# Kernel tuning notes

Hardware: AMD Instinct MI355X
Metric: run time of the kernel (lower is better)

Reference implementation:

```python
import jax, jax.numpy as jnp
import numpy as np
from jax.ops import segment_sum

N = 100000   # nodes
E = 1600000  # edges
D = 128      # node_feature_dim == hidden_dim
DE = 16      # edge_feature_dim
G = 512      # num_graphs
EPS = 1e-5   # BatchNorm eps


def setup_inputs() -> dict:
    key = jax.random.key(0)
    ks = jax.random.split(key, 24)
    inp = {
        "x": jax.random.normal(ks[0], (N, D), jnp.float32),
        "edge_index": jax.random.randint(ks[1], (2, E), 0, N, jnp.int64),
        "batch_idx": jnp.sort(jax.random.randint(ks[2], (N,), 0, G, jnp.int64)),
        "edge_attr": jax.random.normal(ks[3], (E, DE), jnp.float32),
        "num_graphs": G,
    }
    s = 1.0 / np.sqrt(D)
    # GCN layer 1 (D -> D) + BatchNorm1d (eval-mode running stats)
    inp["W1"] = jax.random.normal(ks[4], (D, D), jnp.float32) * s
    inp["b1"] = jnp.zeros((D,), jnp.float32)
    inp["g1"] = jax.random.uniform(ks[5], (D,), jnp.float32, 0.5, 1.5)
    inp["bt1"] = jax.random.normal(ks[6], (D,), jnp.float32) * 0.1
    inp["m1"] = jax.random.normal(ks[7], (D,), jnp.float32) * 0.1
    inp["v1"] = jax.random.uniform(ks[8], (D,), jnp.float32, 0.5, 1.5)
    # GCN layer 2
    inp["W2"] = jax.random.normal(ks[9], (D, D), jnp.float32) * s
    inp["b2"] = jnp.zeros((D,), jnp.float32)
    inp["g2"] = jax.random.uniform(ks[10], (D,), jnp.float32, 0.5, 1.5)
    inp["bt2"] = jax.random.normal(ks[11], (D,), jnp.float32) * 0.1
    inp["m2"] = jax.random.normal(ks[12], (D,), jnp.float32) * 0.1
    inp["v2"] = jax.random.uniform(ks[13], (D,), jnp.float32, 0.5, 1.5)
    # edge encoder: Linear(DE,D) -> ReLU -> Linear(D,D)
    inp["We1"] = jax.random.normal(ks[14], (DE, D), jnp.float32) / np.sqrt(DE)
    inp["be1"] = jnp.zeros((D,), jnp.float32)
    inp["We2"] = jax.random.normal(ks[15], (D, D), jnp.float32) * s
    inp["be2"] = jnp.zeros((D,), jnp.float32)
    return inp


def _gcn_conv(x, W, b, src, dst, n):
    # PyG GCNConv: add self-loops, sym norm D^-1/2 (A+I) D^-1/2, then X W + b
    xw = x @ W  # [n, out]
    loops = jnp.arange(n, dtype=src.dtype)
    s = jnp.concatenate([src, loops])
    d = jnp.concatenate([dst, loops])
    deg = segment_sum(jnp.ones_like(d, dtype=xw.dtype), d, num_segments=n)
    dinv = jnp.where(deg > 0, jax.lax.rsqrt(jnp.maximum(deg, 1.0)), 0.0)
    norm = dinv[s] * dinv[d]  # [e+n]
    msg = xw[s] * norm[:, None]
    return segment_sum(msg, d, num_segments=n) + b


def _bn_relu(x, g, bt, m, v):
    return jax.nn.relu((x - m) * jax.lax.rsqrt(v + EPS) * g + bt)


def reference(x, edge_index, batch_idx, edge_attr, num_graphs,
              W1, b1, g1, bt1, m1, v1,
              W2, b2, g2, bt2, m2, v2,
              We1, be1, We2, be2):
    n = x.shape[0]
    src, dst = edge_index[0], edge_index[1]
    # two GraphConvLayer: GCNConv -> BN(eval) -> ReLU -> Dropout(eval=id)
    h = _bn_relu(_gcn_conv(x, W1, b1, src, dst, n), g1, bt1, m1, v1)
    h = _bn_relu(_gcn_conv(h, W2, b2, src, dst, n), g2, bt2, m2, v2)
    # global mean pool over nodes per graph
    nsum = segment_sum(h, batch_idx, num_segments=num_graphs)
    ncnt = segment_sum(jnp.ones((n,), h.dtype), batch_idx, num_segments=num_graphs)
    graph_repr = nsum / jnp.maximum(ncnt, 1.0)[:, None]
    # edge encoder + per-graph edge mean (fused segment-mean)
    e = jax.nn.relu(edge_attr @ We1 + be1) @ We2 + be2  # [E, D]
    edge_batch = batch_idx[src]
    esum = segment_sum(e, edge_batch, num_segments=num_graphs)
    ecnt = segment_sum(jnp.ones((e.shape[0],), e.dtype), edge_batch, num_segments=num_graphs)
    edge_repr = jnp.where(ecnt[:, None] > 0, esum / jnp.maximum(ecnt, 1.0)[:, None], 0.0)
    return graph_repr + edge_repr
```

## Files before the change

kernel.cpp:

```cpp
#include <hip/hip_runtime.h>

#define N_NODES 100000
#define N_EDGES 1600000
#define D 128
#define DE 16
#define G 512
#define EPSBN 1e-5f
#define ESLICE 4
#define EPB 1024
#define EPT (EPB / 256)
#define SCHUNK 1024
#define NSB ((N_NODES + SCHUNK - 1) / SCHUNK)
#define AGG_CH 16
#define DSHIFT 9
#define DBSZ 512
#define NBKT ((N_NODES + DBSZ - 1) / DBSZ)

typedef __bf16 bf16x8 __attribute__((ext_vector_type(8)));
typedef __bf16 bf16x4 __attribute__((ext_vector_type(4)));
typedef float f32x4 __attribute__((ext_vector_type(4)));

__device__ __forceinline__ float bf_lo(unsigned v) { return __uint_as_float(v << 16); }
__device__ __forceinline__ float bf_hi(unsigned v) { return __uint_as_float(v & 0xffff0000u); }

__global__ void k_init(int* __restrict__ deg, int* __restrict__ ecnt, int* __restrict__ dcnt,
                       float* __restrict__ gcnt, float* __restrict__ gsum,
                       float* __restrict__ esum) {
  int i = blockIdx.x * 256 + threadIdx.x;
  if (i < N_NODES) deg[i] = 1;
  if (i < G) { ecnt[i] = 0; gcnt[i] = 0.f; }
  if (i < NBKT) dcnt[i] = 0;
  if (i < G * D) { gsum[i] = 0.f; esum[i] = 0.f; }
}

__global__ void k_count(const int* __restrict__ ei, const int* __restrict__ batch,
                        int* __restrict__ deg, int* __restrict__ ecnt, int* __restrict__ dcnt) {
  __shared__ int bins[G];
  __shared__ int dbins[NBKT];
  int tid = threadIdx.x;
  for (int i = tid; i < G; i += 256) bins[i] = 0;
  for (int i = tid; i < NBKT; i += 256) dbins[i] = 0;
  __syncthreads();
  int base = blockIdx.x * 4096;
  for (int t = tid; t < 4096; t += 256) {
    int e = base + t;
    if (e < N_EDGES) {
      int s = ei[e];
      int d = ei[N_EDGES + e];
      atomicAdd(&deg[d], 1);
      atomicAdd(&bins[batch[s]], 1);
      atomicAdd(&dbins[d >> DSHIFT], 1);
    }
  }
  __syncthreads();
  for (int i = tid; i < G; i += 256) if (bins[i]) atomicAdd(&ecnt[i], bins[i]);
  for (int i = tid; i < NBKT; i += 256) if (dbins[i]) atomicAdd(&dcnt[i], dbins[i]);
}

__global__ __launch_bounds__(256) void k_scan_part(const int* __restrict__ deg,
                                                   int* __restrict__ part) {
  __shared__ int red[4];
  int tid = threadIdx.x;
  int base = blockIdx.x * SCHUNK + tid * 4;
  int s = 0;
  #pragma unroll
  for (int k = 0; k < 4; ++k) {
    int i = base + k;
    if (i < N_NODES) s += deg[i];
  }
  #pragma unroll
  for (int off = 32; off > 0; off >>= 1) s += __shfl_down(s, off);
  if ((tid & 63) == 0) red[tid >> 6] = s;
  __syncthreads();
  if (tid == 0) part[blockIdx.x] = red[0] + red[1] + red[2] + red[3];
}

__global__ void k_scan_mid(int* __restrict__ part, const int* __restrict__ ecnt,
                           int* __restrict__ ebs, int* __restrict__ ecur_pad,
                           const int* __restrict__ dcnt, int* __restrict__ dbs,
                           int* __restrict__ dcur_pad) {
  __shared__ int sb[512];
  int tid = threadIdx.x;
  int v = (tid < NSB) ? part[tid] : 0;
  sb[tid] = v;
  __syncthreads();
  for (int off = 1; off < 512; off <<= 1) {
    int t = (tid >= off) ? sb[tid - off] : 0;
    __syncthreads();
    sb[tid] += t;
    __syncthreads();
  }
  if (tid < NSB) part[tid] = sb[tid] - v;
  __syncthreads();
  int v2 = ecnt[tid];
  sb[tid] = v2;
  __syncthreads();
  for (int off = 1; off < 512; off <<= 1) {
    int t = (tid >= off) ? sb[tid - off] : 0;
    __syncthreads();
    sb[tid] += t;
    __syncthreads();
  }
  ebs[tid] = sb[tid] - v2;
  ecur_pad[tid * 16] = sb[tid] - v2;
  __syncthreads();
  int v3 = (tid < NBKT) ? dcnt[tid] : 0;
  sb[tid] = v3;
  __syncthreads();
  for (int off = 1; off < 512; off <<= 1) {
    int t = (tid >= off) ? sb[tid - off] : 0;
    __syncthreads();
    sb[tid] += t;
    __syncthreads();
  }
  if (tid < NBKT) { dbs[tid] = sb[tid] - v3; dcur_pad[tid * 16] = sb[tid] - v3; }
}

__global__ __launch_bounds__(256) void k_scan_write(const int* __restrict__ deg,
                                                    const int* __restrict__ part,
                                                    int* __restrict__ rs,
                                                    float* __restrict__ dinv) {
  __shared__ int sb[256];
  int tid = threadIdx.x;
  int base = blockIdx.x * SCHUNK + tid * 4;
  int d[4];
  int s = 0;
  #pragma unroll
  for (int k = 0; k < 4; ++k) {
    int i = base + k;
    d[k] = (i < N_NODES) ? deg[i] : 0;
    s += d[k];
  }
  sb[tid] = s;
  __syncthreads();
  for (int off = 1; off < 256; off <<= 1) {
    int t = (tid >= off) ? sb[tid - off] : 0;
    __syncthreads();
    sb[tid] += t;
    __syncthreads();
  }
  int ex = sb[tid] - s + part[blockIdx.x];
  #pragma unroll
  for (int k = 0; k < 4; ++k) {
    int i = base + k;
    if (i < N_NODES) {
      rs[i] = ex;
      dinv[i] = rsqrtf((float)d[k]);
      ex += d[k];
    }
  }
}

__global__ __launch_bounds__(256) void k_scatter(const int* __restrict__ ei,
                                                 const int* __restrict__ batch,
                                                 int* __restrict__ ecur_pad,
                                                 int* __restrict__ dcur_pad,
                                                 int2* __restrict__ pairs,
                                                 int* __restrict__ idlist) {
  __shared__ int gbins[G];
  __shared__ int gbase[G];
  __shared__ int dbins[NBKT];
  __shared__ int dbase[NBKT];
  __shared__ int gsrc[EPB];
  __shared__ int gdst[EPB];
  __shared__ int dsrc[EPB];
  __shared__ int ddst[EPB];
  int tid = threadIdx.x;
  for (int i = tid; i < G; i += 256) gbins[i] = 0;
  for (int i = tid; i < NBKT; i += 256) dbins[i] = 0;
  __syncthreads();
  int e0 = blockIdx.x * EPB;
  int nvalid = N_EDGES - e0;
  if (nvalid > EPB) nvalid = EPB;
  int ge[EPT], gr[EPT], db[EPT], dr[EPT];
  #pragma unroll
  for (int k = 0; k < EPT; ++k) {
    int e = e0 + k * 256 + tid;
    ge[k] = -1;
    if (e < N_EDGES) {
      int s = ei[e], d = ei[N_EDGES + e];
      int g = batch[s];
      ge[k] = g;
      gr[k] = atomicAdd(&gbins[g], 1);
      db[k] = d >> DSHIFT;
      dr[k] = atomicAdd(&dbins[db[k]], 1);
    }
  }
  __syncthreads();
  for (int i = tid; i < G; i += 256) {
    int cnt = gbins[i];
    gbase[i] = cnt ? atomicAdd(&ecur_pad[i * 16], cnt) : 0;
  }
  for (int i = tid; i < NBKT; i += 256) {
    int cnt = dbins[i];
    dbase[i] = cnt ? atomicAdd(&dcur_pad[i * 16], cnt) : 0;
  }
  int v0 = gbins[tid], v1 = gbins[tid + 256];
  int vd = (tid < NBKT) ? dbins[tid] : 0;
  gsrc[tid] = vd;
  __syncthreads();
  for (int off = 1; off < 512; off <<= 1) {
    int a = (tid >= off) ? gbins[tid - off] : 0;
    int b = gbins[tid + 256 - off];
    int c = (off < 256 && tid >= off) ? gsrc[tid - off] : 0;
    __syncthreads();
    gbins[tid] += a;
    gbins[tid + 256] += b;
    if (off < 256) gsrc[tid] += c;
    __syncthreads();
  }
  gbins[tid] -= v0;
  gbins[tid + 256] -= v1;
  if (tid < NBKT) dbins[tid] = gsrc[tid] - vd;
  __syncthreads();
  #pragma unroll
  for (int k = 0; k < EPT; ++k) {
    if (ge[k] >= 0) {
      int el = k * 256 + tid;
      int g = ge[k];
      int sG = gbins[g] + gr[k];
      gsrc[sG] = el;
      gdst[sG] = gbase[g] + gr[k];
      int bkt = db[k];
      int sD = dbins[bkt] + dr[k];
      dsrc[sD] = el;
      ddst[sD] = dbase[bkt] + dr[k];
    }
  }
  __syncthreads();
  for (int p = tid; p < nvalid; p += 256) {
    idlist[gdst[p]] = e0 + gsrc[p];
  }
  for (int p = tid; p < nvalid; p += 256) {
    int e = e0 + dsrc[p];
    pairs[ddst[p]] = make_int2(ei[e], ei[N_EDGES + e]);
  }
}

__global__ __launch_bounds__(256) void k_scatter_nbr(const int2* __restrict__ pairs,
                                                     const int* __restrict__ dbs,
                                                     const int* __restrict__ dcnt,
                                                     const int* __restrict__ rs,
                                                     int* __restrict__ nbr) {
  __shared__ int cur[DBSZ];
  int tid = threadIdx.x;
  int bkt = blockIdx.x;
  int nodeBase = bkt << DSHIFT;
  for (int l = tid; l < DBSZ; l += 256) {
    int node = nodeBase + l;
    cur[l] = (node < N_NODES) ? rs[node] : 0;
  }
  __syncthreads();
  int start = dbs[bkt], n = dcnt[bkt];
  for (int i = tid; i < n; i += 256) {
    int2 p = pairs[start + i];
    int pos = atomicAdd(&cur[p.y - nodeBase], 1);
    nbr[pos] = p.x;
  }
}

__global__ void k_prep_w(const float* __restrict__ W, __bf16* __restrict__ Wf) {
  int tid = threadIdx.x;
  for (int idx = blockIdx.x * 256 + tid; idx < 16384; idx += 8 * 256) {
    int j = idx & 7;
    int lane = (idx >> 3) & 63;
    int cb = (idx >> 9) & 7;
    int kc = idx >> 12;
    int k = kc * 32 + (lane >> 4) * 8 + j;
    int n = cb * 16 + (lane & 15);
    Wf[idx] = (__bf16)W[k * 128 + n];
  }
}

__global__ __launch_bounds__(256) void k_gemm_mfma(const float* __restrict__ X,
                                                   const __bf16* __restrict__ Wf,
                                                   const float* __restrict__ dinv,
                                                   __bf16* __restrict__ out) {
  __shared__ __bf16 sXb[64][136];
  int tid = threadIdx.x;
  int wave = tid >> 6, lane = tid & 63;
  int m = lane & 15, kg = lane >> 4;
  int base = blockIdx.x * 64;
  #pragma unroll
  for (int i = 0; i < 8; ++i) {
    int idx = tid + i * 256;
    int r = idx >> 5, cq = idx & 31;
    int row = base + r;
    float4 v = make_float4(0.f, 0.f, 0.f, 0.f);
    if (row < N_NODES) v = *(const float4*)(X + (size_t)row * 128 + cq * 4);
    bf16x4 h;
    h[0] = (__bf16)v.x; h[1] = (__bf16)v.y; h[2] = (__bf16)v.z; h[3] = (__bf16)v.w;
    *(bf16x4*)(&sXb[r][cq * 4]) = h;
  }
  __syncthreads();
  int r0 = wave * 16;
  f32x4 acc[8];
  #pragma unroll
  for (int cb = 0; cb < 8; ++cb) acc[cb] = (f32x4){0.f, 0.f, 0.f, 0.f};
  #pragma unroll
  for (int kc = 0; kc < 4; ++kc) {
    bf16x8 afrag = *(const bf16x8*)(&sXb[r0 + m][kc * 32 + kg * 8]);
    #pragma unroll
    for (int cb = 0; cb < 8; ++cb) {
      bf16x8 bfrag = *(const bf16x8*)(Wf + (((size_t)(kc * 8 + cb) * 64 + lane) << 3));
      acc[cb] = __builtin_amdgcn_mfma_f32_16x16x32_bf16(afrag, bfrag, acc[cb], 0, 0, 0);
    }
  }
  #pragma unroll
  for (int r = 0; r < 4; ++r) {
    int grow = base + r0 + kg * 4 + r;
    if (grow < N_NODES) {
      float dv = dinv[grow];
      #pragma unroll
      for (int cb = 0; cb < 8; ++cb)
        out[(size_t)grow * 128 + cb * 16 + m] = (__bf16)(acc[cb][r] * dv);
    }
  }
}

__global__ __launch_bounds__(256) void k_agg_bn(const unsigned* __restrict__ Au,
                                                const int* __restrict__ nbr,
                                                const int* __restrict__ rs,
                                                const int* __restrict__ deg,
                                                const float* __restrict__ dinv,
                                                const float* __restrict__ b,
                                                const float* __restrict__ gm,
                                                const float* __restrict__ bt,
                                                const float* __restrict__ m,
                                                const float* __restrict__ v,
                                                float* __restrict__ outB) {
  int tid = threadIdx.x;
  int wave = tid >> 6, lane = tid & 63;
  int c0 = lane * 2, c1 = c0 + 1;
  float sc0 = gm[c0] * rsqrtf(v[c0] + EPSBN), sc1 = gm[c1] * rsqrtf(v[c1] + EPSBN);
  float sh0 = bt[c0] - m[c0] * sc0, sh1 = bt[c1] - m[c1] * sc1;
  float bb0 = b[c0], bb1 = b[c1];
  int base = (blockIdx.x * 4 + wave) * AGG_CH;
  for (int nn = 0; nn < AGG_CH; ++nn) {
    int i = base + nn;
    if (i >= N_NODES) return;
    unsigned sv = Au[(size_t)i * 64 + lane];
    float s0 = bf_lo(sv), s1 = bf_hi(sv);
    int j = rs[i];
    int end = j + deg[i] - 1;
    for (; j + 3 < end; j += 4) {
      int n0 = nbr[j], n1 = nbr[j + 1], n2 = nbr[j + 2], n3 = nbr[j + 3];
      unsigned a0 = Au[(size_t)n0 * 64 + lane];
      unsigned a1 = Au[(size_t)n1 * 64 + lane];
      unsigned a2 = Au[(size_t)n2 * 64 + lane];
      unsigned a3 = Au[(size_t)n3 * 64 + lane];
      s0 += bf_lo(a0) + bf_lo(a1) + bf_lo(a2) + bf_lo(a3);
      s1 += bf_hi(a0) + bf_hi(a1) + bf_hi(a2) + bf_hi(a3);
    }
    for (; j < end; ++j) {
      unsigned a = Au[(size_t)nbr[j] * 64 + lane];
      s0 += bf_lo(a); s1 += bf_hi(a);
    }
    float dv = dinv[i];
    float y0 = fmaxf((dv * s0 + bb0) * sc0 + sh0, 0.f);
    float y1 = fmaxf((dv * s1 + bb1) * sc1 + sh1, 0.f);
    *(float2*)(outB + (size_t)i * 128 + c0) = make_float2(y0, y1);
  }
}

__global__ __launch_bounds__(256) void k_agg_bn_pool(const unsigned* __restrict__ Au,
                                                     const int* __restrict__ nbr,
                                                     const int* __restrict__ rs,
                                                     const int* __restrict__ deg,
                                                     const float* __restrict__ dinv,
                                                     const int* __restrict__ batch,
                                                     const float* __restrict__ b,
                                                     const float* __restrict__ gm,
                                                     const float* __restrict__ bt,
                                                     const float* __restrict__ m,
                                                     const float* __restrict__ v,
                                                     float* __restrict__ gsum,
                                                     float* __restrict__ gcnt) {
  int tid = threadIdx.x;
  int wave = tid >> 6, lane = tid & 63;
  int c0 = lane * 2, c1 = c0 + 1;
  float sc0 = gm[c0] * rsqrtf(v[c0] + EPSBN), sc1 = gm[c1] * rsqrtf(v[c1] + EPSBN);
  float sh0 = bt[c0] - m[c0] * sc0, sh1 = bt[c1] - m[c1] * sc1;
  float bb0 = b[c0], bb1 = b[c1];
  int base = (blockIdx.x * 4 + wave) * AGG_CH;
  if (base >= N_NODES) return;
  float acc0 = 0.f, acc1 = 0.f, cnt = 0.f;
  int curg = -1;
  for (int nn = 0; nn < AGG_CH; ++nn) {
    int i = base + nn;
    if (i >= N_NODES) break;
    int bg = batch[i];
    if (bg != curg) {
      if (curg >= 0) {
        atomicAdd(&gsum[(size_t)curg * 128 + c0], acc0);
        atomicAdd(&gsum[(size_t)curg * 128 + c1], acc1);
        if (lane == 0) atomicAdd(&gcnt[curg], cnt);
      }
      acc0 = 0.f; acc1 = 0.f; cnt = 0.f; curg = bg;
    }
    unsigned sv = Au[(size_t)i * 64 + lane];
    float s0 = bf_lo(sv), s1 = bf_hi(sv);
    int j = rs[i];
    int end = j + deg[i] - 1;
    for (; j + 3 < end; j += 4) {
      int n0 = nbr[j], n1 = nbr[j + 1], n2 = nbr[j + 2], n3 = nbr[j + 3];
      unsigned a0 = Au[(size_t)n0 * 64 + lane];
      unsigned a1 = Au[(size_t)n1 * 64 + lane];
      unsigned a2 = Au[(size_t)n2 * 64 + lane];
      unsigned a3 = Au[(size_t)n3 * 64 + lane];
      s0 += bf_lo(a0) + bf_lo(a1) + bf_lo(a2) + bf_lo(a3);
      s1 += bf_hi(a0) + bf_hi(a1) + bf_hi(a2) + bf_hi(a3);
    }
    for (; j < end; ++j) {
      unsigned a = Au[(size_t)nbr[j] * 64 + lane];
      s0 += bf_lo(a); s1 += bf_hi(a);
    }
    float dv = dinv[i];
    acc0 += fmaxf((dv * s0 + bb0) * sc0 + sh0, 0.f);
    acc1 += fmaxf((dv * s1 + bb1) * sc1 + sh1, 0.f);
    cnt += 1.f;
  }
  if (curg >= 0) {
    atomicAdd(&gsum[(size_t)curg * 128 + c0], acc0);
    atomicAdd(&gsum[(size_t)curg * 128 + c1], acc1);
    if (lane == 0) atomicAdd(&gcnt[curg], cnt);
  }
}

__global__ __launch_bounds__(256) void k_edge_hidden(
    const float* __restrict__ edge_attr,
    const int* __restrict__ idlist,
    const int* __restrict__ ebs, const int* __restrict__ ecnt,
    const float* __restrict__ We1, const float* __restrict__ be1,
    float* __restrict__ esum) {
  int tid = threadIdx.x;
  int wave = tid >> 6;
  int lane = tid & 63;
  int n = lane & 15;
  int kg = lane >> 4;
  int toff = kg >> 1;
  int cp = kg & 1;
  int g = blockIdx.x / ESLICE;
  int slice = blockIdx.x % ESLICE;

  bf16x8 bfrag[8];
  float biasv[8];
  #pragma unroll
  for (int blk = 0; blk < 8; ++blk) {
    #pragma unroll
    for (int j = 0; j < 8; ++j) {
      int k = kg * 8 + j;
      float w = (k < DE) ? We1[k * 128 + blk * 16 + n] : 0.f;
      bfrag[blk][j] = (__bf16)w;
    }
    biasv[blk] = be1[blk * 16 + n];
  }

  int start = ebs[g], cnt = ecnt[g];
  int lim = start + cnt;
  int ntiles = (cnt + 15) >> 4;
  const int nstream = ESLICE * 4;
  int sid = slice * 4 + wave;
  int tpc = (ntiles + nstream - 1) / nstream;
  int t0 = sid * tpc;
  int t1 = t0 + tpc; if (t1 > ntiles) t1 = ntiles;

  float racc[8] = {0.f, 0.f, 0.f, 0.f, 0.f, 0.f, 0.f, 0.f};

  auto compute_tile = [&](int t, bf16x8 afrag) {
    int jb = start + (t << 4);
    if (jb + 16 <= lim) {
      #pragma unroll
      for (int blk = 0; blk < 8; ++blk) {
        f32x4 acc = {0.f, 0.f, 0.f, 0.f};
        acc = __builtin_amdgcn_mfma_f32_16x16x32_bf16(afrag, bfrag[blk], acc, 0, 0, 0);
        #pragma unroll
        for (int r = 0; r < 4; ++r)
          racc[blk] += fmaxf(acc[r] + biasv[blk], 0.f);
      }
    } else {
      #pragma unroll
      for (int blk = 0; blk < 8; ++blk) {
        f32x4 acc = {0.f, 0.f, 0.f, 0.f};
        acc = __builtin_amdgcn_mfma_f32_16x16x32_bf16(afrag, bfrag[blk], acc, 0, 0, 0);
        #pragma unroll
        for (int r = 0; r < 4; ++r) {
          int rr = kg * 4 + r;
          if (jb + rr < lim) racc[blk] += fmaxf(acc[r] + biasv[blk], 0.f);
        }
      }
    }
  };

  for (int t = t0; t < t1; t += 2) {
    int tt = t + toff;
    int ttc = tt < ntiles ? tt : ntiles - 1;
    int slot = start + (ttc << 4) + n;
    int sc = slot < lim - 1 ? slot : lim - 1;
    int e = idlist[sc];
    const float4* q = (const float4*)(edge_attr + (size_t)e * DE + cp * 8);
    float4 f0 = q[0], f1 = q[1];
    union { bf16x8 v; int i[4]; } mine, swp;
    mine.v[0] = (__bf16)f0.x; mine.v[1] = (__bf16)f0.y;
    mine.v[2] = (__bf16)f0.z; mine.v[3] = (__bf16)f0.w;
    mine.v[4] = (__bf16)f1.x; mine.v[5] = (__bf16)f1.y;
    mine.v[6] = (__bf16)f1.z; mine.v[7] = (__bf16)f1.w;
    #pragma unroll
    for (int w2 = 0; w2 < 4; ++w2) swp.i[w2] = __shfl_xor(mine.i[w2], 32);
    bf16x8 a0 = {}, a1 = {};
    if (kg < 2) { a0 = mine.v; a1 = swp.v; }
    compute_tile(t, a0);
    if (t + 1 < t1) compute_tile(t + 1, a1);
  }

  #pragma unroll
  for (int blk = 0; blk < 8; ++blk) {
    float vsum = racc[blk];
    vsum += __shfl_xor(vsum, 16);
    vsum += __shfl_xor(vsum, 32);
    if (lane < 16) atomicAdd(&esum[(size_t)g * 128 + blk * 16 + n], vsum);
  }
}

__global__ void k_final(const float* __restrict__ esum, const int* __restrict__ ecnt,
                        const float* __restrict__ gsum, const float* __restrict__ gcnt,
                        const float* __restrict__ We2, const float* __restrict__ be2,
                        float* __restrict__ out) {
  __shared__ float mh[128];
  int g = blockIdx.x, c = threadIdx.x;
  int ec = ecnt[g];
  mh[c] = (ec > 0) ? esum[(size_t)g * 128 + c] / (float)ec : 0.f;
  __syncthreads();
  float acc = 0.f;
  #pragma unroll 8
  for (int k = 0; k < 128; ++k) acc += mh[k] * We2[k * 128 + c];
  float er = (ec > 0) ? (acc + be2[c]) : 0.f;
  float gr = gsum[(size_t)g * 128 + c] / fmaxf(gcnt[g], 1.f);
  out[(size_t)g * 128 + c] = gr + er;
}

extern "C" void kernel_launch(void* const* d_in, const int* in_sizes, int n_in,
                              void* d_out, int out_size, void* d_ws, size_t ws_size,
                              hipStream_t stream) {
  const float* x        = (const float*)d_in[0];
  const int*   ei       = (const int*)d_in[1];
  const int*   batch    = (const int*)d_in[2];
  const float* edge_attr= (const float*)d_in[3];
  const float* W1 = (const float*)d_in[5];
  const float* b1 = (const float*)d_in[6];
  const float* g1 = (const float*)d_in[7];
  const float* bt1= (const float*)d_in[8];
  const float* m1 = (const float*)d_in[9];
  const float* v1 = (const float*)d_in[10];
  const float* W2 = (const float*)d_in[11];
  const float* b2 = (const float*)d_in[12];
  const float* g2 = (const float*)d_in[13];
  const float* bt2= (const float*)d_in[14];
  const float* m2 = (const float*)d_in[15];
  const float* v2 = (const float*)d_in[16];
  const float* We1= (const float*)d_in[17];
  const float* be1= (const float*)d_in[18];
  const float* We2= (const float*)d_in[19];
  const float* be2= (const float*)d_in[20];
  float* out = (float*)d_out;

  char* ws = (char*)d_ws;
  size_t off = 0;
  auto take = [&](size_t bytes) -> char* {
    char* p = ws + off;
    off += (bytes + 255) & ~(size_t)255;
    return p;
  };
  __bf16* A       = (__bf16*)take((size_t)N_NODES * 128 * 2);
  float*  B       = (float*) take((size_t)N_NODES * 128 * 4);
  float*  dinv    = (float*) take((size_t)N_NODES * 4);
  int*    deg     = (int*)   take((size_t)N_NODES * 4);
  int*    rs      = (int*)   take((size_t)N_NODES * 4);
  int*    nbr     = (int*)   take((size_t)(N_EDGES + N_NODES) * 4);
  int2*   pairs   = (int2*)  take((size_t)N_EDGES * 8);
  int*    idlist  = (int*)   take((size_t)N_EDGES * 4);
  __bf16* Wf1     = (__bf16*)take((size_t)16384 * 2);
  __bf16* Wf2     = (__bf16*)take((size_t)16384 * 2);
  int*    ecnt    = (int*)   take((size_t)G * 4);
  int*    ebs     = (int*)   take((size_t)G * 4);
  int*    ecur_pad= (int*)   take((size_t)G * 16 * 4);
  int*    dcnt    = (int*)   take((size_t)NBKT * 4);
  int*    dbs     = (int*)   take((size_t)NBKT * 4);
  int*    dcur_pad= (int*)   take((size_t)NBKT * 16 * 4);
  float*  gcnt    = (float*) take((size_t)G * 4);
  float*  esum    = (float*) take((size_t)G * 128 * 4);
  float*  gsum    = (float*) take((size_t)G * 128 * 4);
  int*    part    = (int*)   take((size_t)NSB * 4);

  k_init<<<(N_NODES + 255) / 256, 256, 0, stream>>>(deg, ecnt, dcnt, gcnt, gsum, esum);
  k_prep_w<<<8, 256, 0, stream>>>(W1, Wf1);
  k_prep_w<<<8, 256, 0, stream>>>(W2, Wf2);
  k_count<<<(N_EDGES + 4095) / 4096, 256, 0, stream>>>(ei, batch, deg, ecnt, dcnt);
  k_scan_part<<<NSB, 256, 0, stream>>>(deg, part);
  k_scan_mid<<<1, 512, 0, stream>>>(part, ecnt, ebs, ecur_pad, dcnt, dbs, dcur_pad);
  k_scan_write<<<NSB, 256, 0, stream>>>(deg, part, rs, dinv);
  k_scatter<<<(N_EDGES + EPB - 1) / EPB, 256, 0, stream>>>(ei, batch, ecur_pad, dcur_pad, pairs, idlist);
  k_scatter_nbr<<<NBKT, 256, 0, stream>>>(pairs, dbs, dcnt, rs, nbr);
  const int aggBlocks = (N_NODES + 4 * AGG_CH - 1) / (4 * AGG_CH);
  k_gemm_mfma<<<(N_NODES + 63) / 64, 256, 0, stream>>>(x, Wf1, dinv, A);
  k_agg_bn<<<aggBlocks, 256, 0, stream>>>((const unsigned*)A, nbr, rs, deg, dinv, b1, g1, bt1, m1, v1, B);
  k_gemm_mfma<<<(N_NODES + 63) / 64, 256, 0, stream>>>(B, Wf2, dinv, A);
  k_agg_bn_pool<<<aggBlocks, 256, 0, stream>>>((const unsigned*)A, nbr, rs, deg, dinv, batch, b2, g2, bt2, m2, v2, gsum, gcnt);
  k_edge_hidden<<<G * ESLICE, 256, 0, stream>>>(edge_attr, idlist, ebs, ecnt, We1, be1, esum);
  k_final<<<G, 128, 0, stream>>>(esum, ecnt, gsum, gcnt, We2, be2, out);
}
```

Measured before the change: 693.6 us.

## Co-schedule edge encoder blocks with the two aggregation kernels

The standalone edge-hidden kernel is split into two halves, and each half is appended as extra blocks to the layer-1 and layer-2 aggregation launches, dispatched by block index. This lets the compute-bound MFMA edge encoding overlap with the memory-bound neighbor gathers and removes one kernel launch. The combined kernels may use more registers, since the launch bound is shared by both bodies, which could lower occupancy for the gather blocks.

```diff
diff --git a/kernel.cpp b/kernel.cpp
--- a/kernel.cpp
+++ b/kernel.cpp
@@ -12,6 +12,7 @@
 #define SCHUNK 1024
 #define NSB ((N_NODES + SCHUNK - 1) / SCHUNK)
 #define AGG_CH 16
+#define AGGB ((N_NODES + 4 * AGG_CH - 1) / (4 * AGG_CH))
 #define DSHIFT 9
 #define DBSZ 512
 #define NBKT ((N_NODES + DBSZ - 1) / DBSZ)
@@ -318,24 +319,21 @@
   }
 }
 
-__global__ __launch_bounds__(256) void k_agg_bn(const unsigned* __restrict__ Au,
-                                                const int* __restrict__ nbr,
-                                                const int* __restrict__ rs,
-                                                const int* __restrict__ deg,
-                                                const float* __restrict__ dinv,
-                                                const float* __restrict__ b,
-                                                const float* __restrict__ gm,
-                                                const float* __restrict__ bt,
-                                                const float* __restrict__ m,
-                                                const float* __restrict__ v,
-                                                float* __restrict__ outB) {
+
+__device__ __forceinline__ void agg_bn_body(
+    int blk, const unsigned* __restrict__ Au, const int* __restrict__ nbr,
+    const int* __restrict__ rs, const int* __restrict__ deg,
+    const float* __restrict__ dinv, const float* __restrict__ b,
+    const float* __restrict__ gm, const float* __restrict__ bt,
+    const float* __restrict__ m, const float* __restrict__ v,
+    float* __restrict__ outB) {
   int tid = threadIdx.x;
   int wave = tid >> 6, lane = tid & 63;
   int c0 = lane * 2, c1 = c0 + 1;
   float sc0 = gm[c0] * rsqrtf(v[c0] + EPSBN), sc1 = gm[c1] * rsqrtf(v[c1] + EPSBN);
   float sh0 = bt[c0] - m[c0] * sc0, sh1 = bt[c1] - m[c1] * sc1;
   float bb0 = b[c0], bb1 = b[c1];
-  int base = (blockIdx.x * 4 + wave) * AGG_CH;
+  int base = (blk * 4 + wave) * AGG_CH;
   for (int nn = 0; nn < AGG_CH; ++nn) {
     int i = base + nn;
     if (i >= N_NODES) return;
@@ -363,26 +361,21 @@
   }
 }
 
-__global__ __launch_bounds__(256) void k_agg_bn_pool(const unsigned* __restrict__ Au,
-                                                     const int* __restrict__ nbr,
-                                                     const int* __restrict__ rs,
-                                                     const int* __restrict__ deg,
-                                                     const float* __restrict__ dinv,
-                                                     const int* __restrict__ batch,
-                                                     const float* __restrict__ b,
-                                                     const float* __restrict__ gm,
-                                                     const float* __restrict__ bt,
-                                                     const float* __restrict__ m,
-                                                     const float* __restrict__ v,
-                                                     float* __restrict__ gsum,
-                                                     float* __restrict__ gcnt) {
+__device__ __forceinline__ void agg_bn_pool_body(
+    int blk, const unsigned* __restrict__ Au, const int* __restrict__ nbr,
+    const int* __restrict__ rs, const int* __restrict__ deg,
+    const float* __restrict__ dinv, const int* __restrict__ batch,
+    const float* __restrict__ b, const float* __restrict__ gm,
+    const float* __restrict__ bt, const float* __restrict__ m,
+    const float* __restrict__ v, float* __restrict__ gsum,
+    float* __restrict__ gcnt) {
   int tid = threadIdx.x;
   int wave = tid >> 6, lane = tid & 63;
   int c0 = lane * 2, c1 = c0 + 1;
   float sc0 = gm[c0] * rsqrtf(v[c0] + EPSBN), sc1 = gm[c1] * rsqrtf(v[c1] + EPSBN);
   float sh0 = bt[c0] - m[c0] * sc0, sh1 = bt[c1] - m[c1] * sc1;
   float bb0 = b[c0], bb1 = b[c1];
-  int base = (blockIdx.x * 4 + wave) * AGG_CH;
+  int base = (blk * 4 + wave) * AGG_CH;
   if (base >= N_NODES) return;
   float acc0 = 0.f, acc1 = 0.f, cnt = 0.f;
   int curg = -1;
@@ -427,12 +420,11 @@
   }
 }
 
-__global__ __launch_bounds__(256) void k_edge_hidden(
-    const float* __restrict__ edge_attr,
-    const int* __restrict__ idlist,
-    const int* __restrict__ ebs, const int* __restrict__ ecnt,
-    const float* __restrict__ We1, const float* __restrict__ be1,
-    float* __restrict__ esum) {
+__device__ __forceinline__ void edge_hidden_body(
+    int g, int slice, const float* __restrict__ edge_attr,
+    const int* __restrict__ idlist, const int* __restrict__ ebs,
+    const int* __restrict__ ecnt, const float* __restrict__ We1,
+    const float* __restrict__ be1, float* __restrict__ esum) {
   int tid = threadIdx.x;
   int wave = tid >> 6;
   int lane = tid & 63;
@@ -440,8 +432,6 @@
   int kg = lane >> 4;
   int toff = kg >> 1;
   int cp = kg & 1;
-  int g = blockIdx.x / ESLICE;
-  int slice = blockIdx.x % ESLICE;
 
   bf16x8 bfrag[8];
   float biasv[8];
@@ -519,6 +509,47 @@
     vsum += __shfl_xor(vsum, 16);
     vsum += __shfl_xor(vsum, 32);
     if (lane < 16) atomicAdd(&esum[(size_t)g * 128 + blk * 16 + n], vsum);
+  }
+}
+
+__global__ __launch_bounds__(256) void k_fused_l1(
+    const unsigned* __restrict__ Au, const int* __restrict__ nbr,
+    const int* __restrict__ rs, const int* __restrict__ deg,
+    const float* __restrict__ dinv, const float* __restrict__ b,
+    const float* __restrict__ gm, const float* __restrict__ bt,
+    const float* __restrict__ m, const float* __restrict__ v,
+    float* __restrict__ outB,
+    const float* __restrict__ edge_attr, const int* __restrict__ idlist,
+    const int* __restrict__ ebs, const int* __restrict__ ecnt,
+    const float* __restrict__ We1, const float* __restrict__ be1,
+    float* __restrict__ esum) {
+  int bid = blockIdx.x;
+  if (bid < AGGB) {
+    agg_bn_body(bid, Au, nbr, rs, deg, dinv, b, gm, bt, m, v, outB);
+  } else {
+    int eb = bid - AGGB;
+    edge_hidden_body(eb >> 1, eb & 1, edge_attr, idlist, ebs, ecnt, We1, be1, esum);
+  }
+}
+
+__global__ __launch_bounds__(256) void k_fused_l2(
+    const unsigned* __restrict__ Au, const int* __restrict__ nbr,
+    const int* __restrict__ rs, const int* __restrict__ deg,
+    const float* __restrict__ dinv, const int* __restrict__ batch,
+    const float* __restrict__ b, const float* __restrict__ gm,
+    const float* __restrict__ bt, const float* __restrict__ m,
+    const float* __restrict__ v, float* __restrict__ gsum,
+    float* __restrict__ gcnt,
+    const float* __restrict__ edge_attr, const int* __restrict__ idlist,
+    const int* __restrict__ ebs, const int* __restrict__ ecnt,
+    const float* __restrict__ We1, const float* __restrict__ be1,
+    float* __restrict__ esum) {
+  int bid = blockIdx.x;
+  if (bid < AGGB) {
+    agg_bn_pool_body(bid, Au, nbr, rs, deg, dinv, batch, b, gm, bt, m, v, gsum, gcnt);
+  } else {
+    int eb = bid - AGGB;
+    edge_hidden_body(eb >> 1, 2 + (eb & 1), edge_attr, idlist, ebs, ecnt, We1, be1, esum);
   }
 }
 
@@ -601,11 +632,13 @@
   k_scan_write<<<NSB, 256, 0, stream>>>(deg, part, rs, dinv);
   k_scatter<<<(N_EDGES + EPB - 1) / EPB, 256, 0, stream>>>(ei, batch, ecur_pad, dcur_pad, pairs, idlist);
   k_scatter_nbr<<<NBKT, 256, 0, stream>>>(pairs, dbs, dcnt, rs, nbr);
-  const int aggBlocks = (N_NODES + 4 * AGG_CH - 1) / (4 * AGG_CH);
   k_gemm_mfma<<<(N_NODES + 63) / 64, 256, 0, stream>>>(x, Wf1, dinv, A);
-  k_agg_bn<<<aggBlocks, 256, 0, stream>>>((const unsigned*)A, nbr, rs, deg, dinv, b1, g1, bt1, m1, v1, B);
+  k_fused_l1<<<AGGB + 2 * G, 256, 0, stream>>>((const unsigned*)A, nbr, rs, deg, dinv,
+                                               b1, g1, bt1, m1, v1, B,
+                                               edge_attr, idlist, ebs, ecnt, We1, be1, esum);
   k_gemm_mfma<<<(N_NODES + 63) / 64, 256, 0, stream>>>(B, Wf2, dinv, A);
-  k_agg_bn_pool<<<aggBlocks, 256, 0, stream>>>((const unsigned*)A, nbr, rs, deg, dinv, batch, b2, g2, bt2, m2, v2, gsum, gcnt);
-  k_edge_hidden<<<G * ESLICE, 256, 0, stream>>>(edge_attr, idlist, ebs, ecnt, We1, be1, esum);
+  k_fused_l2<<<AGGB + 2 * G, 256, 0, stream>>>((const unsigned*)A, nbr, rs, deg, dinv, batch,
+                                               b2, g2, bt2, m2, v2, gsum, gcnt,
+                                               edge_attr, idlist, ebs, ecnt, We1, be1, esum);
   k_final<<<G, 128, 0, stream>>>(esum, ecnt, gsum, gcnt, We2, be2, out);
 }
```

Measured after the change: 835.0 us. 1.2x slower.

## Pre-convert edge features to bf16 in count pass and merge setup kernels

Applied to the files above, without the earlier changes.

Edge attributes are now converted to bf16 once, in the streaming count kernel, and stored in a new workspace buffer. The edge-hidden kernel then gathers 16-byte bf16 rows instead of 32-byte fp32 rows for its random idlist accesses, and the lane-to-row mapping is rearranged so each lane loads one half row. The init and the two weight-prep launches are merged into a single setup kernel to cut launch count. The cost is an extra 51 MB write plus a full read of edge_attr in the count kernel.

```diff
diff --git a/kernel.cpp b/kernel.cpp
--- a/kernel.cpp
+++ b/kernel.cpp
@@ -15,6 +15,7 @@
 #define DSHIFT 9
 #define DBSZ 512
 #define NBKT ((N_NODES + DBSZ - 1) / DBSZ)
+#define INITB ((N_NODES + 255) / 256)
 
 typedef __bf16 bf16x8 __attribute__((ext_vector_type(8)));
 typedef __bf16 bf16x4 __attribute__((ext_vector_type(4)));
@@ -23,17 +24,41 @@
 __device__ __forceinline__ float bf_lo(unsigned v) { return __uint_as_float(v << 16); }
 __device__ __forceinline__ float bf_hi(unsigned v) { return __uint_as_float(v & 0xffff0000u); }
 
-__global__ void k_init(int* __restrict__ deg, int* __restrict__ ecnt, int* __restrict__ dcnt,
-                       float* __restrict__ gcnt, float* __restrict__ gsum,
-                       float* __restrict__ esum) {
-  int i = blockIdx.x * 256 + threadIdx.x;
-  if (i < N_NODES) deg[i] = 1;
-  if (i < G) { ecnt[i] = 0; gcnt[i] = 0.f; }
-  if (i < NBKT) dcnt[i] = 0;
-  if (i < G * D) { gsum[i] = 0.f; esum[i] = 0.f; }
+__device__ __forceinline__ void prep_w_body(int pb, const float* __restrict__ W,
+                                            __bf16* __restrict__ Wf) {
+  int tid = threadIdx.x;
+  for (int idx = pb * 256 + tid; idx < 16384; idx += 8 * 256) {
+    int j = idx & 7;
+    int lane = (idx >> 3) & 63;
+    int cb = (idx >> 9) & 7;
+    int kc = idx >> 12;
+    int k = kc * 32 + (lane >> 4) * 8 + j;
+    int n = cb * 16 + (lane & 15);
+    Wf[idx] = (__bf16)W[k * 128 + n];
+  }
+}
+
+__global__ void k_setup(int* __restrict__ deg, int* __restrict__ ecnt, int* __restrict__ dcnt,
+                        float* __restrict__ gcnt, float* __restrict__ gsum,
+                        float* __restrict__ esum,
+                        const float* __restrict__ W1, __bf16* __restrict__ Wf1,
+                        const float* __restrict__ W2, __bf16* __restrict__ Wf2) {
+  int b = blockIdx.x;
+  if (b < INITB) {
+    int i = b * 256 + threadIdx.x;
+    if (i < N_NODES) deg[i] = 1;
+    if (i < G) { ecnt[i] = 0; gcnt[i] = 0.f; }
+    if (i < NBKT) dcnt[i] = 0;
+    if (i < G * D) { gsum[i] = 0.f; esum[i] = 0.f; }
+  } else if (b < INITB + 8) {
+    prep_w_body(b - INITB, W1, Wf1);
+  } else {
+    prep_w_body(b - INITB - 8, W2, Wf2);
+  }
 }
 
 __global__ void k_count(const int* __restrict__ ei, const int* __restrict__ batch,
+                        const float* __restrict__ edge_attr, __bf16* __restrict__ eaB,
                         int* __restrict__ deg, int* __restrict__ ecnt, int* __restrict__ dcnt) {
   __shared__ int bins[G];
   __shared__ int dbins[NBKT];
@@ -50,6 +75,15 @@
       atomicAdd(&deg[d], 1);
       atomicAdd(&bins[batch[s]], 1);
       atomicAdd(&dbins[d >> DSHIFT], 1);
+      const float4* p = (const float4*)(edge_attr + (size_t)e * DE);
+      float4 f0 = p[0], f1 = p[1], f2 = p[2], f3 = p[3];
+      bf16x8 h0, h1;
+      h0[0] = (__bf16)f0.x; h0[1] = (__bf16)f0.y; h0[2] = (__bf16)f0.z; h0[3] = (__bf16)f0.w;
+      h0[4] = (__bf16)f1.x; h0[5] = (__bf16)f1.y; h0[6] = (__bf16)f1.z; h0[7] = (__bf16)f1.w;
+      h1[0] = (__bf16)f2.x; h1[1] = (__bf16)f2.y; h1[2] = (__bf16)f2.z; h1[3] = (__bf16)f2.w;
+      h1[4] = (__bf16)f3.x; h1[5] = (__bf16)f3.y; h1[6] = (__bf16)f3.z; h1[7] = (__bf16)f3.w;
+      bf16x8* q = (bf16x8*)(eaB + (size_t)e * DE);
+      q[0] = h0; q[1] = h1;
     }
   }
   __syncthreads();
@@ -256,19 +290,6 @@
     int2 p = pairs[start + i];
     int pos = atomicAdd(&cur[p.y - nodeBase], 1);
     nbr[pos] = p.x;
-  }
-}
-
-__global__ void k_prep_w(const float* __restrict__ W, __bf16* __restrict__ Wf) {
-  int tid = threadIdx.x;
-  for (int idx = blockIdx.x * 256 + tid; idx < 16384; idx += 8 * 256) {
-    int j = idx & 7;
-    int lane = (idx >> 3) & 63;
-    int cb = (idx >> 9) & 7;
-    int kc = idx >> 12;
-    int k = kc * 32 + (lane >> 4) * 8 + j;
-    int n = cb * 16 + (lane & 15);
-    Wf[idx] = (__bf16)W[k * 128 + n];
   }
 }
 
@@ -428,7 +449,7 @@
 }
 
 __global__ __launch_bounds__(256) void k_edge_hidden(
-    const float* __restrict__ edge_attr,
+    const __bf16* __restrict__ eaB,
     const int* __restrict__ idlist,
     const int* __restrict__ ebs, const int* __restrict__ ecnt,
     const float* __restrict__ We1, const float* __restrict__ be1,
@@ -438,8 +459,8 @@
   int lane = tid & 63;
   int n = lane & 15;
   int kg = lane >> 4;
-  int toff = kg >> 1;
-  int cp = kg & 1;
+  int rowIdx = (lane & 15) + ((lane >> 5) << 4);
+  int half = (lane >> 4) & 1;
   int g = blockIdx.x / ESLICE;
   int slice = blockIdx.x % ESLICE;
 
@@ -493,18 +514,11 @@
   };
 
   for (int t = t0; t < t1; t += 2) {
-    int tt = t + toff;
-    int ttc = tt < ntiles ? tt : ntiles - 1;
-    int slot = start + (ttc << 4) + n;
+    int slot = start + (t << 4) + rowIdx;
     int sc = slot < lim - 1 ? slot : lim - 1;
     int e = idlist[sc];
-    const float4* q = (const float4*)(edge_attr + (size_t)e * DE + cp * 8);
-    float4 f0 = q[0], f1 = q[1];
     union { bf16x8 v; int i[4]; } mine, swp;
-    mine.v[0] = (__bf16)f0.x; mine.v[1] = (__bf16)f0.y;
-    mine.v[2] = (__bf16)f0.z; mine.v[3] = (__bf16)f0.w;
-    mine.v[4] = (__bf16)f1.x; mine.v[5] = (__bf16)f1.y;
-    mine.v[6] = (__bf16)f1.z; mine.v[7] = (__bf16)f1.w;
+    mine.v = *(const bf16x8*)(eaB + (size_t)e * DE + half * 8);
     #pragma unroll
     for (int w2 = 0; w2 < 4; ++w2) swp.i[w2] = __shfl_xor(mine.i[w2], 32);
     bf16x8 a0 = {}, a1 = {};
@@ -579,6 +593,7 @@
   int*    nbr     = (int*)   take((size_t)(N_EDGES + N_NODES) * 4);
   int2*   pairs   = (int2*)  take((size_t)N_EDGES * 8);
   int*    idlist  = (int*)   take((size_t)N_EDGES * 4);
+  __bf16* eaB     = (__bf16*)take((size_t)N_EDGES * DE * 2);
   __bf16* Wf1     = (__bf16*)take((size_t)16384 * 2);
   __bf16* Wf2     = (__bf16*)take((size_t)16384 * 2);
   int*    ecnt    = (int*)   take((size_t)G * 4);
@@ -592,10 +607,10 @@
   float*  gsum    = (float*) take((size_t)G * 128 * 4);
   int*    part    = (int*)   take((size_t)NSB * 4);
 
-  k_init<<<(N_NODES + 255) / 256, 256, 0, stream>>>(deg, ecnt, dcnt, gcnt, gsum, esum);
-  k_prep_w<<<8, 256, 0, stream>>>(W1, Wf1);
-  k_prep_w<<<8, 256, 0, stream>>>(W2, Wf2);
-  k_count<<<(N_EDGES + 4095) / 4096, 256, 0, stream>>>(ei, batch, deg, ecnt, dcnt);
+  k_setup<<<INITB + 16, 256, 0, stream>>>(deg, ecnt, dcnt, gcnt, gsum, esum,
+                                          W1, Wf1, W2, Wf2);
+  k_count<<<(N_EDGES + 4095) / 4096, 256, 0, stream>>>(ei, batch, edge_attr, eaB,
+                                                       deg, ecnt, dcnt);
   k_scan_part<<<NSB, 256, 0, stream>>>(deg, part);
   k_scan_mid<<<1, 512, 0, stream>>>(part, ecnt, ebs, ecur_pad, dcnt, dbs, dcur_pad);
   k_scan_write<<<NSB, 256, 0, stream>>>(deg, part, rs, dinv);
@@ -606,6 +621,6 @@
   k_agg_bn<<<aggBlocks, 256, 0, stream>>>((const unsigned*)A, nbr, rs, deg, dinv, b1, g1, bt1, m1, v1, B);
   k_gemm_mfma<<<(N_NODES + 63) / 64, 256, 0, stream>>>(B, Wf2, dinv, A);
   k_agg_bn_pool<<<aggBlocks, 256, 0, stream>>>((const unsigned*)A, nbr, rs, deg, dinv, batch, b2, g2, bt2, m2, v2, gsum, gcnt);
-  k_edge_hidden<<<G * ESLICE, 256, 0, stream>>>(edge_attr, idlist, ebs, ecnt, We1, be1, esum);
+  k_edge_hidden<<<G * ESLICE, 256, 0, stream>>>(eaB, idlist, ebs, ecnt, We1, be1, esum);
   k_final<<<G, 128, 0, stream>>>(esum, ecnt, gsum, gcnt, We2, be2, out);
 }
```

Result: no change. 690.7 us (-0.4%).
